# Kernel tuning notes

Hardware: AMD Instinct MI355X
Metric: run time of the kernel (lower is better)

The kernel has to match this reference:

```python
import jax, jax.numpy as jnp
import numpy as np

ALPHA = 0.25
GAMMA = 2.0
LAMBDA_T = 0.1


def count_components(fg):
    """Count 6-connected components per volume. fg: [M,H,W,D] bool.
    Min-label propagation + pointer jumping (parallel union-find style CCL),
    matching scipy.ndimage.label's default face-connectivity structure.
    Returns float32 [M] component counts."""
    M, H, W, D = fg.shape
    N = H * W * D
    BIG = jnp.int32(N)  # sentinel label for background / padding
    idx = jnp.arange(N, dtype=jnp.int32).reshape(1, H, W, D)
    L0 = jnp.broadcast_to(idx, fg.shape)

    def shift(a, axis, d):
        # b[i] = a[i-d] along `axis`, padded with BIG outside the volume
        pad = [(0, 0)] * 4
        pad[axis] = (max(d, 0), max(-d, 0))
        ap = jnp.pad(a, pad, constant_values=N)
        sl = [slice(None)] * 4
        sl[axis] = slice(max(-d, 0), max(-d, 0) + a.shape[axis])
        return ap[tuple(sl)]

    def one_step(L):
        Lv = jnp.where(fg, L, BIG)
        m = Lv
        for ax in (1, 2, 3):
            for d in (1, -1):
                m = jnp.minimum(m, shift(Lv, ax, d))
        Ln = jnpp_min = jnp.where(fg, jnp.minimum(L, m), L)
        # pointer jumping (L <- L[L]) twice for log-depth convergence
        Lf = Ln.reshape(M, N)
        Lf = jnp.take_along_axis(Lf, Lf, axis=1)
        Lf = jnp.take_along_axis(Lf, Lf, axis=1)
        return Lf.reshape(M, H, W, D)

    def cond(s):
        return s[1]

    def body(s):
        L, _ = s
        Ln = one_step(L)
        return (Ln, jnp.any(Ln != L))

    L, _ = jax.lax.while_loop(cond, body, (L0, jnp.bool_(True)))
    # at fixed point every foreground component carries its min linear index;
    # roots satisfy L[i] == i
    roots = fg & (L == idx)
    return jnp.sum(roots, axis=(1, 2, 3)).astype(jnp.float32)


def _focal(x, t):
    p = jax.nn.sigmoid(x)
    pt = jnp.where(t == 1, p, 1.0 - p)
    bce = jax.nn.softplus(x) - x * t  # BCE-with-logits, elementwise
    alpha_t = jnp.where(t == 1, ALPHA, 1.0 - ALPHA)
    return jnp.mean(alpha_t * (1.0 - pt) ** GAMMA * bce)


def _topology(x, t):
    B, C = x.shape[:2]
    spatial = x.shape[2:]
    fg_p = (jax.nn.sigmoid(x) > 0.5).reshape(B * C, *spatial)
    fg_t = (t > 0.5).reshape(B * C, *spatial)
    cc_p = count_components(fg_p).reshape(B, C).mean(axis=0)  # mean over batch per class
    cc_t = count_components(fg_t).reshape(B, C).mean(axis=0)
    return jnp.mean(jnp.abs(cc_p - cc_t))  # sum over classes / C


def setup_inputs() -> dict:
    key = jax.random.key(0)
    k1, k2 = jax.random.split(key)
    shape = (2, 2, 96, 96, 96)
    pred_logits = jax.random.normal(k1, shape, dtype=jnp.float32)
    target_binary = jax.random.randint(k2, shape, 0, 2).astype(jnp.float32)
    return {"pred_logits": pred_logits, "target_binary": target_binary}


def reference(pred_logits, target_binary):
    focal = _focal(pred_logits, target_binary)
    topo = jax.lax.stop_gradient(_topology(pred_logits, target_binary))
    return focal + LAMBDA_T * topo
```

## Files before the change

### kernel.cpp

```cpp
#include <hip/hip_runtime.h>
#include <math.h>

#define N_VOX (96*96*96)
#define NVOL 8
#define NEL (4*N_VOX)
#define PLANE (96*96)

#define TW 8
#define TH 8
#define TILES_W 12
#define TILES_H 12
#define TILE_VOX (96*TW*TH)
#define TILE_WORDS (TILE_VOX/32)
#define MAXRUNS 3072

#define NBPLANES 11
#define NPAIRS (2*NBPLANES)
#define FACES_PER_VOL (2*NPAIRS*PLANE)
#define MAXR 40192
#define FALLR 65536
#define SEGCAP 4608
#define HT2N 4096
#define MAX_PROBES 16

#define WS_ACC   0
#define WS_ROOT  256
#define WS_COMP  1536
#define WS_DONE  2816
#define WS_VDONE 3840
#define WS_PCNT  4096
#define WS_HDR   8192

__device__ __forceinline__ int uf_find(int* __restrict__ L, int x) {
    int r = x;
    int p = L[r];
    while (p != r) { r = p; p = L[r]; }
    if (r != x) atomicMin(&L[x], r);
    return r;
}

__device__ __forceinline__ int uf_merge(int* __restrict__ L, int l1, int l2) {
    int ev = 0;
    while (l1 != l2) {
        if (l1 < l2) { int t = l1; l1 = l2; l2 = t; }
        int l3 = atomicMin(&L[l1], l2);
        if (l3 == l1) { ev++; l1 = l2; }
        else l1 = l3;
    }
    return ev;
}

__device__ __forceinline__ void merge_local(int* lab, int l1, int l2) {
    while (l1 != l2 && l1 != lab[l1]) l1 = lab[l1];
    while (l1 != l2 && l2 != lab[l2]) l2 = lab[l2];
    while (l1 != l2) {
        if (l1 < l2) { int t = l1; l1 = l2; l2 = t; }
        int l3 = atomicMin(&lab[l1], l2);
        l1 = (l3 == l1) ? l2 : l3;
    }
}

__device__ __forceinline__ int rrank(const unsigned* __restrict__ sm,
                                     const int* __restrict__ wpf, int i) {
    int w = i >> 5, b = i & 31;
    unsigned mask = (2u << b) - 1u;
    return wpf[w] + __popc(sm[w] & mask) - 1;
}

__global__ __launch_bounds__(256) void ccl_local(const float* __restrict__ pred,
                                                 const float* __restrict__ targ,
                                                 unsigned short* __restrict__ faces,
                                                 int* __restrict__ rootcnt,
                                                 float* __restrict__ acc,
                                                 int vbase) {
    __shared__ int      lab[MAXRUNS];
    __shared__ unsigned fm[TILE_WORDS];
    __shared__ unsigned sm[TILE_WORDS];
    __shared__ int      wpf[TILE_WORDS];
    __shared__ float fws[4];
    __shared__ int   iws[4];
    __shared__ int   gbase;

    int vloc = blockIdx.y;
    int v = vbase + vloc;
    int tile = blockIdx.x;
    int tw = tile % TILES_W, th = tile / TILES_W;
    int w0 = tw * TW, h0 = th * TH;
    int tbase = h0 * PLANE + w0 * 96;
    unsigned short* Fw = faces + (size_t)vloc * FACES_PER_VOL;
    unsigned short* Fh = Fw + 2 * NBPLANES * PLANE;

    float fsum = 0.0f;
    for (int it = 0; it < TILE_VOX / 256; it++) {
        int i = it * 256 + threadIdx.x;
        int lh = i / 768;
        int j = tbase + i + lh * 8448;
        bool f;
        if (v < 4) {
            float xv = pred[(size_t)v * N_VOX + j];
            float tv = targ[(size_t)v * N_VOX + j];
            f = xv > 0.0f;
            float m   = (tv == 1.0f) ? -xv : xv;
            float at  = (tv == 1.0f) ? 0.25f : 0.75f;
            float e   = __expf(-fabsf(m));
            float inv = 1.0f / (1.0f + e);
            float sig = inv * ((m >= 0.0f) ? 1.0f : e);
            float sp  = fmaxf(m, 0.0f) + __logf(1.0f + e);
            fsum += at * sig * sig * sp;
        } else {
            f = targ[(size_t)(v - 4) * N_VOX + j] > 0.5f;
        }
        unsigned long long bal = __ballot(f);
        if ((threadIdx.x & 63) == 0) {
            fm[i >> 5]       = (unsigned)bal;
            fm[(i >> 5) + 1] = (unsigned)(bal >> 32);
        }
    }
    __syncthreads();

    int cnt = 0;
    {
        unsigned st = 0;
        if (threadIdx.x < TILE_WORDS) {
            unsigned m = fm[threadIdx.x];
            unsigned carry = (threadIdx.x % 3) ? (fm[threadIdx.x - 1] >> 31) : 0u;
            st = m & ~((m << 1) | carry);
            sm[threadIdx.x] = st;
            cnt = __popc(st);
        }
    }
    int inc = cnt;
    for (int off = 1; off < 64; off <<= 1) {
        int u = __shfl_up(inc, off, 64);
        if ((threadIdx.x & 63) >= off) inc += u;
    }
    int wid = threadIdx.x >> 6;
    if ((threadIdx.x & 63) == 63) iws[wid] = inc;
    for (int r = threadIdx.x; r < MAXRUNS; r += 256) lab[r] = r;
    __syncthreads();
    int woff = 0;
    for (int k = 0; k < wid; k++) woff += iws[k];
    if (threadIdx.x < TILE_WORDS) wpf[threadIdx.x] = woff + inc - cnt;
    int Nr = iws[0] + iws[1] + iws[2];
    __syncthreads();

    for (int t = threadIdx.x; t < 336; t += 256) {
        bool wdirn = t < 168;
        int tt = wdirn ? t : t - 168;
        int lh, lw, k;
        if (wdirn) { lh = tt / 21; int rem = tt % 21; lw = rem / 3; k = rem % 3; }
        else       { lh = tt / 24; int rem = tt % 24; lw = rem / 3; k = rem % 3; }
        int wb = (lh * 8 + lw) * 3 + k;
        int nb = wb + (wdirn ? 3 : 24);
        unsigned ov = fm[wb] & fm[nb];
        if (!ov) continue;
        unsigned carry = (k > 0) ? ((fm[wb - 1] & fm[nb - 1]) >> 31) : 0u;
        unsigned starts = ov & ~((ov << 1) | carry);
        int base_i = wb << 5;
        int dir = wdirn ? 96 : 768;
        while (starts) {
            int b = __builtin_ctz(starts);
            starts &= starts - 1;
            int i = base_i + b;
            merge_local(lab, rrank(sm, wpf, i), rrank(sm, wpf, i + dir));
        }
    }
    __syncthreads();

    int myroots = 0;
    for (int r = threadIdx.x; r < Nr; r += 256)
        if (lab[r] == r) myroots++;
    int s = myroots;
    for (int off = 1; off < 64; off <<= 1) {
        int u = __shfl_up(s, off, 64);
        if ((threadIdx.x & 63) >= off) s += u;
    }
    if ((threadIdx.x & 63) == 63) iws[wid] = s;
    __syncthreads();
    int wbase = 0;
    for (int k = 0; k < wid; k++) wbase += iws[k];
    if (threadIdx.x == 0)
        gbase = atomicAdd(&rootcnt[v << 5], iws[0] + iws[1] + iws[2] + iws[3]);
    __syncthreads();
    int nid = gbase + wbase + (s - myroots);
    for (int r = threadIdx.x; r < Nr; r += 256)
        if (lab[r] == r) lab[r] = ~(nid++);
    __syncthreads();

    for (int r = threadIdx.x; r < Nr; r += 256) {
        int p = lab[r];
        if (p >= 0) {
            int q2 = lab[p];
            while (q2 >= 0) { p = q2; q2 = lab[p]; }
            lab[r] = q2;
        }
    }
    __syncthreads();

    for (int t = threadIdx.x; t < 768; t += 256) {
        int f  = t / 192;
        int g  = t % 192;
        int u  = g / 24;
        int d4 = (g % 24) * 4;
        int i0; unsigned short* dst;
        if (f == 0) {
            if (tw == 0) continue;
            i0  = u * 768 + d4;
            dst = Fw + ((tw - 1) * 2 + 1) * PLANE + (h0 + u) * 96 + d4;
        } else if (f == 1) {
            if (tw == TILES_W - 1) continue;
            i0  = u * 768 + 7 * 96 + d4;
            dst = Fw + (tw * 2) * PLANE + (h0 + u) * 96 + d4;
        } else if (f == 2) {
            if (th == 0) continue;
            i0  = u * 96 + d4;
            dst = Fh + ((th - 1) * 2 + 1) * PLANE + (w0 + u) * 96 + d4;
        } else {
            if (th == TILES_H - 1) continue;
            i0  = 7 * 768 + u * 96 + d4;
            dst = Fh + (th * 2) * PLANE + (w0 + u) * 96 + d4;
        }
        unsigned mw = fm[i0 >> 5];
        unsigned short vals[4];
        bool prevf = false;
        for (int q = 0; q < 4; q++) {
            bool fb = (mw >> ((d4 & 31) + q)) & 1;
            if (fb) vals[q] = prevf ? vals[q - 1]
                                    : (unsigned short)(~lab[rrank(sm, wpf, i0 + q)]);
            else vals[q] = 0xFFFFu;
            prevf = fb;
        }
        *(ushort4*)dst = make_ushort4(vals[0], vals[1], vals[2], vals[3]);
    }

    for (int off = 32; off; off >>= 1) fsum += __shfl_down(fsum, off, 64);
    if ((threadIdx.x & 63) == 0) fws[wid] = fsum;
    __syncthreads();
    if (threadIdx.x == 0) {
        float ft = fws[0] + fws[1] + fws[2] + fws[3];
        if (v < 4 && ft != 0.0f) atomicAdd(acc, ft);
    }
}

__global__ __launch_bounds__(1024) void ccl_bmerge(const unsigned short* __restrict__ faces,
                                                   unsigned* __restrict__ pairs,
                                                   int* __restrict__ pcnt,
                                                   int* __restrict__ gfall,
                                                   const int* __restrict__ rootcnt,
                                                   int* __restrict__ comp,
                                                   int* __restrict__ done,
                                                   int* __restrict__ vdone,
                                                   const float* __restrict__ acc,
                                                   float* __restrict__ out,
                                                   int vbase) {
    __shared__ int slab[MAXR];
    __shared__ int offs[NPAIRS + 1];
    __shared__ int wsum[16];
    __shared__ int nloc, lastf, lastv;
    unsigned* ht = (unsigned*)slab;

    int f    = blockIdx.x;
    int vloc = blockIdx.y;
    int v    = vbase + vloc;
    const unsigned short* A = faces + (size_t)vloc * FACES_PER_VOL
                                    + (size_t)(2 * f) * PLANE;
    const unsigned short* B = A + PLANE;
    unsigned* pb = pairs + ((size_t)vloc * NPAIRS + f) * SEGCAP;

    for (int i = threadIdx.x; i < HT2N; i += 1024) ht[i] = 0xFFFFFFFFu;
    if (threadIdx.x == 0) nloc = 0;
    __syncthreads();

    const int GPP = PLANE / 8;
    for (int g = threadIdx.x; g < GPP; g += 1024) {
        int e8 = g * 8;
        int4 aw = *(const int4*)(A + e8);
        int4 bw = *(const int4*)(B + e8);
        unsigned a32[4] = {(unsigned)aw.x, (unsigned)aw.y, (unsigned)aw.z, (unsigned)aw.w};
        unsigned b32[4] = {(unsigned)bw.x, (unsigned)bw.y, (unsigned)bw.z, (unsigned)bw.w};
        bool pf = false;
        if (e8 % 96) pf = (A[e8 - 1] != 0xFFFFu) && (B[e8 - 1] != 0xFFFFu);
        #pragma unroll
        for (int q = 0; q < 8; q++) {
            unsigned av = (a32[q >> 1] >> ((q & 1) * 16)) & 0xFFFFu;
            unsigned bv = (b32[q >> 1] >> ((q & 1) * 16)) & 0xFFFFu;
            bool f2 = (av != 0xFFFFu) && (bv != 0xFFFFu);
            if (f2 && !pf && av != bv) {
                unsigned lo = av < bv ? av : bv;
                unsigned hi = av < bv ? bv : av;
                unsigned key = (lo << 16) | hi;
                unsigned h = (key * 2654435761u) >> 20;
                bool fresh = false;
                for (int pr = 0; pr < MAX_PROBES; pr++) {
                    unsigned prev = atomicCAS(&ht[h], 0xFFFFFFFFu, key);
                    if (prev == 0xFFFFFFFFu) { fresh = true; break; }
                    if (prev == key) break;
                    h = (h + 1) & (HT2N - 1);
                    if (pr == MAX_PROBES - 1) fresh = true;
                }
                if (fresh) {
                    int ix = atomicAdd(&nloc, 1);
                    pb[ix] = key;
                }
            }
            pf = f2;
        }
    }
    __syncthreads();
    if (threadIdx.x == 0) {
        pcnt[v * NPAIRS + f] = nloc;
        __threadfence();
        int old = atomicAdd(&done[v << 5], 1);
        lastf = (old == NPAIRS - 1);
    }
    __syncthreads();
    if (!lastf) return;

    __threadfence();
    int R = rootcnt[v << 5];
    int* lab = (R <= MAXR) ? slab : (gfall + (size_t)vloc * FALLR);
    if (threadIdx.x == 0) {
        int o = 0;
        for (int k = 0; k < NPAIRS; k++) { offs[k] = o; o += pcnt[v * NPAIRS + k]; }
        offs[NPAIRS] = o;
    }
    __syncthreads();
    for (int i = threadIdx.x; i < R; i += 1024) lab[i] = i;
    int tot = offs[NPAIRS];
    __syncthreads();

    int ev = 0;
    for (int gi = threadIdx.x; gi < tot; gi += 1024) {
        int fi = 0;
        while (offs[fi + 1] <= gi) fi++;
        unsigned key = pairs[((size_t)vloc * NPAIRS + fi) * SEGCAP + (gi - offs[fi])];
        int a = (int)(key >> 16), b = (int)(key & 0xFFFFu);
        int ra = uf_find(lab, a);
        int rb = uf_find(lab, b);
        if (ra != rb) ev += uf_merge(lab, ra, rb);
    }

    for (int off = 32; off; off >>= 1) ev += __shfl_down(ev, off, 64);
    if ((threadIdx.x & 63) == 0) wsum[threadIdx.x >> 6] = ev;
    __syncthreads();
    if (threadIdx.x == 0) {
        int tote = 0;
        for (int k = 0; k < 16; k++) tote += wsum[k];
        comp[v << 5] = R - tote;
        __threadfence();
        int old2 = atomicAdd(vdone, 1);
        lastv = (old2 == NVOL - 1);
    }
    __syncthreads();
    if (!lastv) return;

    if (threadIdx.x == 0) {
        __threadfence();
        float c[NVOL];
        for (int w = 0; w < NVOL; w++) c[w] = (float)comp[w << 5];
        float dp0 = 0.5f * (c[0] + c[2]);
        float dp1 = 0.5f * (c[1] + c[3]);
        float dt0 = 0.5f * (c[4] + c[6]);
        float dt1 = 0.5f * (c[5] + c[7]);
        float topo = 0.5f * (fabsf(dp0 - dt0) + fabsf(dp1 - dt1));
        out[0] = acc[0] / (float)NEL + 0.1f * topo;
    }
}

extern "C" void kernel_launch(void* const* d_in, const int* in_sizes, int n_in,
                              void* d_out, int out_size, void* d_ws, size_t ws_size,
                              hipStream_t stream) {
    const float* pred = (const float*)d_in[0];
    const float* targ = (const float*)d_in[1];
    float* out = (float*)d_out;

    float* acc     = (float*)((char*)d_ws + WS_ACC);
    int*   rootcnt = (int*)((char*)d_ws + WS_ROOT);
    int*   comp    = (int*)((char*)d_ws + WS_COMP);
    int*   done    = (int*)((char*)d_ws + WS_DONE);
    int*   vdone   = (int*)((char*)d_ws + WS_VDONE);
    int*   pcnt    = (int*)((char*)d_ws + WS_PCNT);
    unsigned short* faces = (unsigned short*)((char*)d_ws + WS_HDR);

    size_t per_vol = (size_t)FACES_PER_VOL * 2
                   + (size_t)NPAIRS * SEGCAP * 4
                   + (size_t)FALLR * 4;
    size_t avail   = (ws_size > WS_HDR) ? ws_size - WS_HDR : 0;
    int vols_per_pass = (int)(avail / per_vol);
    if (vols_per_pass > NVOL) vols_per_pass = NVOL;
    if (vols_per_pass < 1) vols_per_pass = 1;
    unsigned* pairs = (unsigned*)(faces + (size_t)vols_per_pass * FACES_PER_VOL);
    int* gfall = (int*)(pairs + (size_t)vols_per_pass * NPAIRS * SEGCAP);

    hipMemsetAsync(d_ws, 0, WS_HDR, stream);

    for (int vbase = 0; vbase < NVOL; vbase += vols_per_pass) {
        int nv = NVOL - vbase;
        if (nv > vols_per_pass) nv = vols_per_pass;
        dim3 tgrid(TILES_W * TILES_H, nv);
        ccl_local<<<tgrid, dim3(256), 0, stream>>>(pred, targ, faces,
                                                   rootcnt, acc, vbase);
        dim3 mgrid(NPAIRS, nv);
        ccl_bmerge<<<mgrid, dim3(1024), 0, stream>>>(faces, pairs, pcnt, gfall,
                                                     rootcnt, comp, done, vdone,
                                                     acc, out, vbase);
    }
}
```

Measured before the change: 151.9 us.

## Split foreground bitmask and focal loss into a separate streaming kernel

Adds a pre-pass kernel that reads pred and target with float4 loads, computes the focal loss sum, and packs both foreground masks into global bitmasks. The local CCL tiles then load compact bit words instead of re-reading floats with ballots, and pred is read once instead of per tile pass. The focal accumulator is spread across eight padded slots to reduce atomic contention. This adds an extra kernel launch and a global bitmask buffer in the workspace.

```diff
diff --git a/kernel.cpp b/kernel.cpp
--- a/kernel.cpp
+++ b/kernel.cpp
@@ -5,6 +5,7 @@
 #define NVOL 8
 #define NEL (4*N_VOX)
 #define PLANE (96*96)
+#define GMWORDS (N_VOX/32)
 
 #define TW 8
 #define TH 8
@@ -24,11 +25,11 @@
 #define MAX_PROBES 16
 
 #define WS_ACC   0
-#define WS_ROOT  256
-#define WS_COMP  1536
-#define WS_DONE  2816
-#define WS_VDONE 3840
-#define WS_PCNT  4096
+#define WS_ROOT  1024
+#define WS_COMP  2048
+#define WS_DONE  3072
+#define WS_VDONE 4096
+#define WS_PCNT  4352
 #define WS_HDR   8192
 
 __device__ __forceinline__ int uf_find(int* __restrict__ L, int x) {
@@ -67,17 +68,58 @@
     return wpf[w] + __popc(sm[w] & mask) - 1;
 }
 
-__global__ __launch_bounds__(256) void ccl_local(const float* __restrict__ pred,
-                                                 const float* __restrict__ targ,
+__global__ __launch_bounds__(256) void fgmask_focal(const float* __restrict__ pred,
+                                                    const float* __restrict__ targ,
+                                                    unsigned* __restrict__ gmask,
+                                                    float* __restrict__ acc) {
+    __shared__ float fws[4];
+    int tid = blockIdx.x * 256 + threadIdx.x;
+    int v = tid / GMWORDS;
+    int w = tid - v * GMWORDS;
+    const float4* P = (const float4*)(pred + (size_t)v * N_VOX + w * 32);
+    const float4* T = (const float4*)(targ + (size_t)v * N_VOX + w * 32);
+    unsigned pb = 0, tb = 0;
+    float fsum = 0.0f;
+    #pragma unroll
+    for (int j4 = 0; j4 < 8; j4++) {
+        float4 p4 = P[j4];
+        float4 t4 = T[j4];
+        float pv[4] = {p4.x, p4.y, p4.z, p4.w};
+        float tv[4] = {t4.x, t4.y, t4.z, t4.w};
+        #pragma unroll
+        for (int q = 0; q < 4; q++) {
+            int j = j4 * 4 + q;
+            if (pv[q] > 0.0f)  pb |= (1u << j);
+            if (tv[q] > 0.5f)  tb |= (1u << j);
+            float m   = (tv[q] == 1.0f) ? -pv[q] : pv[q];
+            float at  = (tv[q] == 1.0f) ? 0.25f : 0.75f;
+            float e   = __expf(-fabsf(m));
+            float inv = 1.0f / (1.0f + e);
+            float sig = inv * ((m >= 0.0f) ? 1.0f : e);
+            float sp  = fmaxf(m, 0.0f) + __logf(1.0f + e);
+            fsum += at * sig * sig * sp;
+        }
+    }
+    gmask[(size_t)v * GMWORDS + w]       = pb;
+    gmask[(size_t)(v + 4) * GMWORDS + w] = tb;
+
+    for (int off = 32; off; off >>= 1) fsum += __shfl_down(fsum, off, 64);
+    if ((threadIdx.x & 63) == 0) fws[threadIdx.x >> 6] = fsum;
+    __syncthreads();
+    if (threadIdx.x == 0) {
+        float ft = fws[0] + fws[1] + fws[2] + fws[3];
+        if (ft != 0.0f) atomicAdd(&acc[(blockIdx.x & 7) << 5], ft);
+    }
+}
+
+__global__ __launch_bounds__(256) void ccl_local(const unsigned* __restrict__ gmask,
                                                  unsigned short* __restrict__ faces,
                                                  int* __restrict__ rootcnt,
-                                                 float* __restrict__ acc,
                                                  int vbase) {
     __shared__ int      lab[MAXRUNS];
     __shared__ unsigned fm[TILE_WORDS];
     __shared__ unsigned sm[TILE_WORDS];
     __shared__ int      wpf[TILE_WORDS];
-    __shared__ float fws[4];
     __shared__ int   iws[4];
     __shared__ int   gbase;
 
@@ -89,33 +131,14 @@
     int tbase = h0 * PLANE + w0 * 96;
     unsigned short* Fw = faces + (size_t)vloc * FACES_PER_VOL;
     unsigned short* Fh = Fw + 2 * NBPLANES * PLANE;
-
-    float fsum = 0.0f;
-    for (int it = 0; it < TILE_VOX / 256; it++) {
-        int i = it * 256 + threadIdx.x;
-        int lh = i / 768;
-        int j = tbase + i + lh * 8448;
-        bool f;
-        if (v < 4) {
-            float xv = pred[(size_t)v * N_VOX + j];
-            float tv = targ[(size_t)v * N_VOX + j];
-            f = xv > 0.0f;
-            float m   = (tv == 1.0f) ? -xv : xv;
-            float at  = (tv == 1.0f) ? 0.25f : 0.75f;
-            float e   = __expf(-fabsf(m));
-            float inv = 1.0f / (1.0f + e);
-            float sig = inv * ((m >= 0.0f) ? 1.0f : e);
-            float sp  = fmaxf(m, 0.0f) + __logf(1.0f + e);
-            fsum += at * sig * sig * sp;
-        } else {
-            f = targ[(size_t)(v - 4) * N_VOX + j] > 0.5f;
-        }
-        unsigned long long bal = __ballot(f);
-        if ((threadIdx.x & 63) == 0) {
-            fm[i >> 5]       = (unsigned)bal;
-            fm[(i >> 5) + 1] = (unsigned)(bal >> 32);
-        }
-    }
+    const unsigned* gm = gmask + (size_t)v * GMWORDS;
+
+    if (threadIdx.x < TILE_WORDS) {
+        int t = threadIdx.x;
+        int lh = t / 24, rem = t % 24;
+        fm[t] = gm[(tbase >> 5) + lh * 288 + rem];
+    }
+    for (int r = threadIdx.x; r < MAXRUNS; r += 256) lab[r] = r;
     __syncthreads();
 
     int cnt = 0;
@@ -136,7 +159,6 @@
     }
     int wid = threadIdx.x >> 6;
     if ((threadIdx.x & 63) == 63) iws[wid] = inc;
-    for (int r = threadIdx.x; r < MAXRUNS; r += 256) lab[r] = r;
     __syncthreads();
     int woff = 0;
     for (int k = 0; k < wid; k++) woff += iws[k];
@@ -231,14 +253,6 @@
             prevf = fb;
         }
         *(ushort4*)dst = make_ushort4(vals[0], vals[1], vals[2], vals[3]);
-    }
-
-    for (int off = 32; off; off >>= 1) fsum += __shfl_down(fsum, off, 64);
-    if ((threadIdx.x & 63) == 0) fws[wid] = fsum;
-    __syncthreads();
-    if (threadIdx.x == 0) {
-        float ft = fws[0] + fws[1] + fws[2] + fws[3];
-        if (v < 4 && ft != 0.0f) atomicAdd(acc, ft);
     }
 }
 
@@ -356,6 +370,8 @@
 
     if (threadIdx.x == 0) {
         __threadfence();
+        float fa = 0.0f;
+        for (int a2 = 0; a2 < 8; a2++) fa += acc[a2 << 5];
         float c[NVOL];
         for (int w = 0; w < NVOL; w++) c[w] = (float)comp[w << 5];
         float dp0 = 0.5f * (c[0] + c[2]);
@@ -363,7 +379,7 @@
         float dt0 = 0.5f * (c[4] + c[6]);
         float dt1 = 0.5f * (c[5] + c[7]);
         float topo = 0.5f * (fabsf(dp0 - dt0) + fabsf(dp1 - dt1));
-        out[0] = acc[0] / (float)NEL + 0.1f * topo;
+        out[0] = fa / (float)NEL + 0.1f * topo;
     }
 }
 
@@ -380,12 +396,14 @@
     int*   done    = (int*)((char*)d_ws + WS_DONE);
     int*   vdone   = (int*)((char*)d_ws + WS_VDONE);
     int*   pcnt    = (int*)((char*)d_ws + WS_PCNT);
-    unsigned short* faces = (unsigned short*)((char*)d_ws + WS_HDR);
+    unsigned* gmask = (unsigned*)((char*)d_ws + WS_HDR);
+    unsigned short* faces = (unsigned short*)(gmask + (size_t)NVOL * GMWORDS);
 
     size_t per_vol = (size_t)FACES_PER_VOL * 2
                    + (size_t)NPAIRS * SEGCAP * 4
                    + (size_t)FALLR * 4;
-    size_t avail   = (ws_size > WS_HDR) ? ws_size - WS_HDR : 0;
+    size_t fixed   = WS_HDR + (size_t)NVOL * GMWORDS * 4;
+    size_t avail   = (ws_size > fixed) ? ws_size - fixed : 0;
     int vols_per_pass = (int)(avail / per_vol);
     if (vols_per_pass > NVOL) vols_per_pass = NVOL;
     if (vols_per_pass < 1) vols_per_pass = 1;
@@ -394,12 +412,14 @@
 
     hipMemsetAsync(d_ws, 0, WS_HDR, stream);
 
+    fgmask_focal<<<dim3(4 * GMWORDS / 256), dim3(256), 0, stream>>>(pred, targ,
+                                                                    gmask, acc);
+
     for (int vbase = 0; vbase < NVOL; vbase += vols_per_pass) {
         int nv = NVOL - vbase;
         if (nv > vols_per_pass) nv = vols_per_pass;
         dim3 tgrid(TILES_W * TILES_H, nv);
-        ccl_local<<<tgrid, dim3(256), 0, stream>>>(pred, targ, faces,
-                                                   rootcnt, acc, vbase);
+        ccl_local<<<tgrid, dim3(256), 0, stream>>>(gmask, faces, rootcnt, vbase);
         dim3 mgrid(NPAIRS, nv);
         ccl_bmerge<<<mgrid, dim3(1024), 0, stream>>>(faces, pairs, pcnt, gfall,
                                                      rootcnt, comp, done, vdone,
```

Result: no change. 153.0 us (+0.7%).
